# Kernel optimization log

Hardware: AMD Instinct MI355X
Metric: run time of the kernel (lower is better)

The kernel has to match this reference:

```python
import jax, jax.numpy as jnp
import numpy as np

N = 50000        # nodes
E_RAND = 800000  # random edges (self-loops appended)
H = 4            # heads
F_IN, D1, D2 = 128, 64, 64
MLP_H, NCLS = 200, 2
NEG_SLOPE = 0.2
EPS = 1e-5


def setup_inputs() -> dict:
    key = jax.random.key(0)
    ks = jax.random.split(key, 18)
    p = lambda k, shape: (jax.random.normal(k, shape, jnp.float32) * 0.05)
    features = jax.random.normal(ks[0], (N, F_IN), jnp.float32)
    loops = jnp.arange(N, dtype=jnp.int32)
    src = jnp.concatenate([jax.random.randint(ks[1], (E_RAND,), 0, N, jnp.int32), loops])
    dst = jnp.concatenate([jax.random.randint(ks[2], (E_RAND,), 0, N, jnp.int32), loops])
    return {
        "features": features, "src": src, "dst": dst,
        "W1": p(ks[3], (F_IN, H * D1)), "al1": p(ks[4], (H, D1)), "ar1": p(ks[5], (H, D1)), "b1": p(ks[6], (H * D1,)),
        "W2": p(ks[7], (D1, H * D2)), "al2": p(ks[8], (H, D2)), "ar2": p(ks[9], (H, D2)), "b2": p(ks[10], (H * D2,)),
        "Wm1": p(ks[11], (D2, MLP_H)), "bm1": p(ks[12], (MLP_H,)),
        "gamma": jnp.ones((MLP_H,), jnp.float32), "beta": jnp.zeros((MLP_H,), jnp.float32),
        "Wm2": p(ks[13], (MLP_H, NCLS)), "bm2": p(ks[14], (NCLS,)),
    }


def gat_layer(x, W, al, ar, b, src, dst):
    # x: [N, F]; W: [F, H*D]
    Hh, D = al.shape
    h = (x @ W).reshape(N, Hh, D)                      # [N,H,D]
    el = jnp.einsum('nhd,hd->nh', h, al)               # [N,H]
    er = jnp.einsum('nhd,hd->nh', h, ar)               # [N,H]
    e = jax.nn.leaky_relu(el[src] + er[dst], NEG_SLOPE)  # [E,H]
    # edge softmax over incoming edges of each dst node
    m = jax.ops.segment_max(e, dst, num_segments=N)    # [N,H]
    ex = jnp.exp(e - m[dst])
    s = jax.ops.segment_sum(ex, dst, num_segments=N)   # [N,H]
    a = ex / s[dst]                                    # [E,H]
    out = jax.ops.segment_sum(a[:, :, None] * h[src], dst, num_segments=N)  # [N,H,D]
    out = jax.nn.relu(out + b.reshape(1, Hh, D))
    return out.mean(axis=1)                            # mean over heads -> [N,D]


def reference(features, src, dst, W1, al1, ar1, b1, W2, al2, ar2, b2,
              Wm1, bm1, gamma, beta, Wm2, bm2):
    h = gat_layer(features, W1, al1, ar1, b1, src, dst)   # dropout = identity (eval)
    h = gat_layer(h, W2, al2, ar2, b2, src, dst)
    # MLPPredictor: Dropout(id) -> Linear -> ReLU -> BatchNorm1d (batch stats) -> Linear
    z = jax.nn.relu(h @ Wm1 + bm1)                        # [N, MLP_H]
    mu = z.mean(axis=0)
    var = ((z - mu) ** 2).mean(axis=0)                    # biased var (torch BN)
    z = (z - mu) * jax.lax.rsqrt(var + EPS) * gamma + beta
    return z @ Wm2 + bm2                                  # [N, NCLS]
```

## Files before the change

### kernel.cpp

```cpp
#include <hip/hip_runtime.h>
#include <hip/hip_bf16.h>

#define NNODES 50000
#define MLP_HID 200
#define NB_SCAN 196

#define NB_CONV 6250
#define NB_W1   256
#define NB_W2   256
#define NB_ZC   196
#define INIT_BLOCKS (NB_CONV + NB_W1 + NB_W2 + NB_ZC + 1)

typedef __attribute__((ext_vector_type(8))) short bf16x8;
typedef __attribute__((ext_vector_type(4))) float f32x4;

__device__ __forceinline__ unsigned short f2bf(float x){
    unsigned u = __float_as_uint(x);
    unsigned r = (u + 0x7fffu + ((u >> 16) & 1u)) >> 16;
    return (unsigned short)r;
}
__device__ __forceinline__ float bflo(unsigned u){ return __uint_as_float(u << 16); }
__device__ __forceinline__ float bfhi(unsigned u){ return __uint_as_float(u & 0xffff0000u); }

__global__ __launch_bounds__(256) void init_all(
    const float* __restrict__ feat, unsigned short* __restrict__ featbf,
    const float* __restrict__ W1, unsigned short* __restrict__ W1T,
    const float* __restrict__ W2, unsigned short* __restrict__ W2T,
    int* __restrict__ cnt, float* __restrict__ bn_acc )
{
    const int b = blockIdx.x, tid = threadIdx.x;
    if (b < NB_CONV){
        long i = ((long)b * 256 + tid) * 4;
        float4 v = *(const float4*)&feat[i];
        ushort4 p;
        p.x = f2bf(v.x); p.y = f2bf(v.y); p.z = f2bf(v.z); p.w = f2bf(v.w);
        *(ushort4*)&featbf[i] = p;
    } else if (b < NB_CONV + NB_W1){
        int c = b - NB_CONV;
        if (tid < 128) W1T[(size_t)c * 128 + tid] = f2bf(W1[(size_t)tid * 256 + c]);
    } else if (b < NB_CONV + NB_W1 + NB_W2){
        int c = b - NB_CONV - NB_W1;
        if (tid < 64) W2T[(size_t)c * 64 + tid] = f2bf(W2[(size_t)tid * 256 + c]);
    } else if (b < NB_CONV + NB_W1 + NB_W2 + NB_ZC){
        int i = (b - NB_CONV - NB_W1 - NB_W2) * 256 + tid;
        if (i < NNODES) cnt[i] = 0;
    } else {
        if (tid < 2 * MLP_HID - 256) bn_acc[256 + tid] = 0.f;
        bn_acc[tid] = 0.f;
    }
}

template<int K>
__global__ __launch_bounds__(256) void mfma_gemm_attn(
    const unsigned short* __restrict__ Abf,
    const unsigned short* __restrict__ WT,
    const float* __restrict__ al, const float* __restrict__ ar,
    unsigned short* __restrict__ hb,
    float* __restrict__ el, float* __restrict__ er, int M)
{
    const int wv = threadIdx.x >> 6, lane = threadIdx.x & 63;
    const int r0 = blockIdx.x * 64 + wv * 16;
    const int l15 = lane & 15, ks = lane >> 4;

    f32x4 acc[16];
    #pragma unroll
    for (int nt = 0; nt < 16; nt++)
        #pragma unroll
        for (int q = 0; q < 4; q++) acc[nt][q] = 0.f;

    const int arow = min(r0 + l15, M - 1);
    const unsigned short* aptr = Abf + (size_t)arow * K + ks * 8;
    const unsigned short* bptr = WT + (size_t)l15 * K + ks * 8;

    #pragma unroll
    for (int k0 = 0; k0 < K; k0 += 32){
        bf16x8 a = *(const bf16x8*)(aptr + k0);
        #pragma unroll
        for (int nt = 0; nt < 16; nt++){
            bf16x8 b = *(const bf16x8*)(bptr + (size_t)nt * 16 * K + k0);
            acc[nt] = __builtin_amdgcn_mfma_f32_16x16x32_bf16(a, b, acc[nt], 0, 0, 0);
        }
    }

    float elv[4][4], erv[4][4];
    #pragma unroll
    for (int r = 0; r < 4; r++)
        #pragma unroll
        for (int hh = 0; hh < 4; hh++){ elv[r][hh] = 0.f; erv[r][hh] = 0.f; }

    #pragma unroll
    for (int nt = 0; nt < 16; nt++){
        int col = nt * 16 + l15;
        float alv = al[col], arv = ar[col];
        #pragma unroll
        for (int reg = 0; reg < 4; reg++){
            elv[reg][nt >> 2] = fmaf(acc[nt][reg], alv, elv[reg][nt >> 2]);
            erv[reg][nt >> 2] = fmaf(acc[nt][reg], arv, erv[reg][nt >> 2]);
        }
    }
    #pragma unroll
    for (int o = 8; o > 0; o >>= 1){
        #pragma unroll
        for (int reg = 0; reg < 4; reg++)
            #pragma unroll
            for (int hh = 0; hh < 4; hh++){
                elv[reg][hh] += __shfl_xor(elv[reg][hh], o);
                erv[reg][hh] += __shfl_xor(erv[reg][hh], o);
            }
    }
    if (l15 == 0){
        #pragma unroll
        for (int reg = 0; reg < 4; reg++){
            int r = r0 + ks * 4 + reg;
            if (r < M){
                #pragma unroll
                for (int hh = 0; hh < 4; hh++){
                    el[r * 4 + hh] = elv[reg][hh];
                    er[r * 4 + hh] = erv[reg][hh];
                }
            }
        }
    }

    __shared__ __align__(16) unsigned short hbuf[4][16][264];
    #pragma unroll
    for (int nt = 0; nt < 16; nt++)
        #pragma unroll
        for (int reg = 0; reg < 4; reg++)
            hbuf[wv][ks * 4 + reg][nt * 16 + l15] = f2bf(acc[nt][reg]);
    #pragma unroll
    for (int t = 0; t < 8; t++){
        int chunk = t * 64 + lane;
        int rr = chunk >> 5;
        int cc = (chunk & 31) * 8;
        int r = r0 + rr;
        if (r < M){
            uint4 v = *(const uint4*)&hbuf[wv][rr][cc];
            *(uint4*)&hb[(size_t)r * 256 + cc] = v;
        }
    }
}

template<int KT, bool RELU, bool BN>
__global__ __launch_bounds__(256) void gemm_tile(const float* __restrict__ A,
                                                 const float* __restrict__ B,
                                                 const float* __restrict__ bias,
                                                 float* __restrict__ C,
                                                 float* __restrict__ bn_sum,
                                                 float* __restrict__ bn_sumsq,
                                                 int M, int Nc){
    __shared__ float As[16][64];
    __shared__ float Bs[16][64];
    __shared__ float bnred[16][64];
    const int tid = threadIdx.x;
    const int tx = tid & 15, ty = tid >> 4;
    const int r0 = blockIdx.y * 64, c0 = blockIdx.x * 64;
    float acc[4][4] = {};
    const int lr  = tid >> 2,  lk4 = (tid & 3) * 4;
    const int bk  = tid >> 4,  bc4 = (tid & 15) * 4;

    for (int k0 = 0; k0 < KT; k0 += 16){
        float4 av = make_float4(0.f,0.f,0.f,0.f);
        if (r0 + lr < M) av = *(const float4*)&A[(size_t)(r0 + lr) * KT + k0 + lk4];
        As[lk4+0][lr] = av.x; As[lk4+1][lr] = av.y;
        As[lk4+2][lr] = av.z; As[lk4+3][lr] = av.w;

        if (c0 + bc4 + 3 < Nc){
            float4 bv = *(const float4*)&B[(size_t)(k0 + bk) * Nc + c0 + bc4];
            Bs[bk][bc4+0] = bv.x; Bs[bk][bc4+1] = bv.y;
            Bs[bk][bc4+2] = bv.z; Bs[bk][bc4+3] = bv.w;
        } else {
            #pragma unroll
            for (int j = 0; j < 4; j++){
                int c = c0 + bc4 + j;
                Bs[bk][bc4+j] = (c < Nc) ? B[(size_t)(k0 + bk) * Nc + c] : 0.f;
            }
        }
        __syncthreads();
        #pragma unroll
        for (int kk = 0; kk < 16; kk++){
            float4 a = *(const float4*)&As[kk][ty*4];
            float4 b = *(const float4*)&Bs[kk][tx*4];
            float arr[4] = {a.x,a.y,a.z,a.w};
            float brr[4] = {b.x,b.y,b.z,b.w};
            #pragma unroll
            for (int i = 0; i < 4; i++)
                #pragma unroll
                for (int j = 0; j < 4; j++)
                    acc[i][j] = fmaf(arr[i], brr[j], acc[i][j]);
        }
        __syncthreads();
    }

    float cs[4] = {0,0,0,0}, css[4] = {0,0,0,0};
    #pragma unroll
    for (int i = 0; i < 4; i++){
        int r = r0 + ty*4 + i;
        bool rok = r < M;
        #pragma unroll
        for (int j = 0; j < 4; j++){
            int c = c0 + tx*4 + j;
            if (c >= Nc) continue;
            float v = acc[i][j];
            if (bias) v += bias[c];
            if (RELU) v = fmaxf(v, 0.f);
            if (rok){
                C[(size_t)r * Nc + c] = v;
                if (BN){ cs[j] += v; css[j] += v * v; }
            }
        }
    }
    if (BN){
        #pragma unroll
        for (int j = 0; j < 4; j++) bnred[ty][tx*4+j] = cs[j];
        __syncthreads();
        if (tid < 64){
            float s = 0.f;
            #pragma unroll
            for (int t = 0; t < 16; t++) s += bnred[t][tid];
            if (c0 + tid < Nc) atomicAdd(&bn_sum[c0 + tid], s);
        }
        __syncthreads();
        #pragma unroll
        for (int j = 0; j < 4; j++) bnred[ty][tx*4+j] = css[j];
        __syncthreads();
        if (tid < 64){
            float s = 0.f;
            #pragma unroll
            for (int t = 0; t < 16; t++) s += bnred[t][tid];
            if (c0 + tid < Nc) atomicAdd(&bn_sumsq[c0 + tid], s);
        }
    }
}

__global__ __launch_bounds__(256) void csr_count(const int* __restrict__ dst,
                                                 int* __restrict__ cnt, int E){
    int e = blockIdx.x * blockDim.x + threadIdx.x;
    if (e < E) atomicAdd(&cnt[dst[e]], 1);
}

__global__ __launch_bounds__(256) void csr_bsum(const int* __restrict__ cnt,
                                                int* __restrict__ bsum){
    __shared__ int red[256];
    int i = blockIdx.x * 256 + threadIdx.x;
    red[threadIdx.x] = (i < NNODES) ? cnt[i] : 0;
    __syncthreads();
    for (int off = 128; off > 0; off >>= 1){
        if (threadIdx.x < off) red[threadIdx.x] += red[threadIdx.x + off];
        __syncthreads();
    }
    if (threadIdx.x == 0) bsum[blockIdx.x] = red[0];
}

__global__ __launch_bounds__(256) void csr_bscan(const int* __restrict__ bsum,
                                                 int* __restrict__ boff){
    __shared__ int part[256];
    int t = threadIdx.x;
    int v = (t < NB_SCAN) ? bsum[t] : 0;
    part[t] = v;
    __syncthreads();
    for (int off = 1; off < 256; off <<= 1){
        int u = (t >= off) ? part[t - off] : 0;
        __syncthreads();
        part[t] += u;
        __syncthreads();
    }
    if (t < NB_SCAN) boff[t] = part[t] - v;
}

__global__ __launch_bounds__(256) void csr_fill(const int* __restrict__ cnt,
                                                const int* __restrict__ boff,
                                                int* __restrict__ row_ptr,
                                                int* __restrict__ cursor){
    __shared__ int part[256];
    int b = blockIdx.x, t = threadIdx.x;
    int i = b * 256 + t;
    int c = (i < NNODES) ? cnt[i] : 0;
    part[t] = c;
    __syncthreads();
    for (int off = 1; off < 256; off <<= 1){
        int u = (t >= off) ? part[t - off] : 0;
        __syncthreads();
        part[t] += u;
        __syncthreads();
    }
    int excl = part[t] - c + boff[b];
    if (i < NNODES){ row_ptr[i] = excl; cursor[i] = excl; }
    if (i == NNODES - 1) row_ptr[NNODES] = excl + c;
}

__global__ __launch_bounds__(256) void csr_scatter(const int* __restrict__ src,
                                                   const int* __restrict__ dst,
                                                   int* __restrict__ cursor,
                                                   int* __restrict__ col_src, int E){
    int e = blockIdx.x * blockDim.x + threadIdx.x;
    if (e >= E) return;
    int pos = atomicAdd(&cursor[dst[e]], 1);
    col_src[pos] = src[e];
}

__global__ __launch_bounds__(256) void gat_edge_v5(
    const int* __restrict__ row_ptr, const int* __restrict__ col_src,
    const float* __restrict__ el, const float* __restrict__ er,
    const unsigned short* __restrict__ hb, const float* __restrict__ bias,
    float* __restrict__ out_f, unsigned short* __restrict__ out_b)
{
    __shared__ float s_w[4][512];
    __shared__ int   s_idx[512];
    __shared__ float s_part[4][4];
    __shared__ float s_inv[4];
    __shared__ __align__(16) float s_red[4][264];
    __shared__ float s_val[256];

    const int n = blockIdx.x;
    const int tid = threadIdx.x;
    const int lane = tid & 63;
    const int wv = tid >> 6;
    const int rs = row_ptr[n], re = row_ptr[n + 1];
    const int K = re - rs;
    const float4 ern = *(const float4*)&er[n * 4];

    float ls0 = 0.f, ls1 = 0.f, ls2 = 0.f, ls3 = 0.f;
    for (int k = tid; k < K; k += 256){
        int s = col_src[rs + k];
        float4 e4 = *(const float4*)&el[s * 4];
        float e0 = e4.x + ern.x; e0 = (e0 >= 0.f) ? e0 : 0.2f * e0;
        float e1 = e4.y + ern.y; e1 = (e1 >= 0.f) ? e1 : 0.2f * e1;
        float e2 = e4.z + ern.z; e2 = (e2 >= 0.f) ? e2 : 0.2f * e2;
        float e3 = e4.w + ern.w; e3 = (e3 >= 0.f) ? e3 : 0.2f * e3;
        float w0 = __expf(e0), w1 = __expf(e1), w2 = __expf(e2), w3 = __expf(e3);
        if (k < 512){
            s_idx[k] = s;
            s_w[0][k] = w0; s_w[1][k] = w1; s_w[2][k] = w2; s_w[3][k] = w3;
        }
        ls0 += w0; ls1 += w1; ls2 += w2; ls3 += w3;
    }
    #pragma unroll
    for (int o = 32; o > 0; o >>= 1){
        ls0 += __shfl_xor(ls0, o); ls1 += __shfl_xor(ls1, o);
        ls2 += __shfl_xor(ls2, o); ls3 += __shfl_xor(ls3, o);
    }
    if (lane == 0){
        s_part[wv][0] = ls0; s_part[wv][1] = ls1;
        s_part[wv][2] = ls2; s_part[wv][3] = ls3;
    }
    __syncthreads();
    if (tid < 4)
        s_inv[tid] = 1.f / (s_part[0][tid] + s_part[1][tid] + s_part[2][tid] + s_part[3][tid]);
    __syncthreads();

    float acc[8];
    #pragma unroll
    for (int q = 0; q < 8; q++) acc[q] = 0.f;
    const int slot = tid >> 5;
    const int c8   = (tid & 31) * 8;
    const int hc   = c8 >> 6;

    for (int kc = 0; kc < K; kc += 512){
        if (kc > 0){
            __syncthreads();
            int kend = min(K, kc + 512);
            for (int k = kc + tid; k < kend; k += 256){
                int s = col_src[rs + k];
                float4 e4 = *(const float4*)&el[s * 4];
                float e0 = e4.x + ern.x; e0 = (e0 >= 0.f) ? e0 : 0.2f * e0;
                float e1 = e4.y + ern.y; e1 = (e1 >= 0.f) ? e1 : 0.2f * e1;
                float e2 = e4.z + ern.z; e2 = (e2 >= 0.f) ? e2 : 0.2f * e2;
                float e3 = e4.w + ern.w; e3 = (e3 >= 0.f) ? e3 : 0.2f * e3;
                int kk = k - kc;
                s_idx[kk] = s;
                s_w[0][kk] = __expf(e0); s_w[1][kk] = __expf(e1);
                s_w[2][kk] = __expf(e2); s_w[3][kk] = __expf(e3);
            }
            __syncthreads();
        }
        int rem = min(512, K - kc);
        int j = slot;
        for (; j + 8 < rem; j += 16){
            int s0 = s_idx[j], s1 = s_idx[j + 8];
            float w0 = s_w[hc][j], w1 = s_w[hc][j + 8];
            uint4 v0 = *(const uint4*)&hb[(size_t)s0 * 256 + c8];
            uint4 v1 = *(const uint4*)&hb[(size_t)s1 * 256 + c8];
            acc[0] = fmaf(w0, bflo(v0.x), acc[0]);
            acc[1] = fmaf(w0, bfhi(v0.x), acc[1]);
            acc[2] = fmaf(w0, bflo(v0.y), acc[2]);
            acc[3] = fmaf(w0, bfhi(v0.y), acc[3]);
            acc[4] = fmaf(w0, bflo(v0.z), acc[4]);
            acc[5] = fmaf(w0, bfhi(v0.z), acc[5]);
            acc[6] = fmaf(w0, bflo(v0.w), acc[6]);
            acc[7] = fmaf(w0, bfhi(v0.w), acc[7]);
            acc[0] = fmaf(w1, bflo(v1.x), acc[0]);
            acc[1] = fmaf(w1, bfhi(v1.x), acc[1]);
            acc[2] = fmaf(w1, bflo(v1.y), acc[2]);
            acc[3] = fmaf(w1, bfhi(v1.y), acc[3]);
            acc[4] = fmaf(w1, bflo(v1.z), acc[4]);
            acc[5] = fmaf(w1, bfhi(v1.z), acc[5]);
            acc[6] = fmaf(w1, bflo(v1.w), acc[6]);
            acc[7] = fmaf(w1, bfhi(v1.w), acc[7]);
        }
        if (j < rem){
            int sN = s_idx[j];
            float w = s_w[hc][j];
            uint4 v = *(const uint4*)&hb[(size_t)sN * 256 + c8];
            acc[0] = fmaf(w, bflo(v.x), acc[0]);
            acc[1] = fmaf(w, bfhi(v.x), acc[1]);
            acc[2] = fmaf(w, bflo(v.y), acc[2]);
            acc[3] = fmaf(w, bfhi(v.y), acc[3]);
            acc[4] = fmaf(w, bflo(v.z), acc[4]);
            acc[5] = fmaf(w, bfhi(v.z), acc[5]);
            acc[6] = fmaf(w, bflo(v.w), acc[6]);
            acc[7] = fmaf(w, bfhi(v.w), acc[7]);
        }
    }
    const float invh = s_inv[hc];
    #pragma unroll
    for (int q = 0; q < 8; q++) acc[q] = acc[q] * invh + __shfl_xor(acc[q] * invh, 32);

    if ((tid & 32) == 0){
        *(float4*)&s_red[slot >> 1][c8]     = make_float4(acc[0], acc[1], acc[2], acc[3]);
        *(float4*)&s_red[slot >> 1][c8 + 4] = make_float4(acc[4], acc[5], acc[6], acc[7]);
    }
    __syncthreads();
    {
        int d = tid;
        float v = s_red[0][d] + s_red[1][d] + s_red[2][d] + s_red[3][d];
        v = fmaxf(v + bias[d], 0.f);
        s_val[d] = v;
    }
    __syncthreads();
    if (tid < 64){
        float m = (s_val[tid] + s_val[tid + 64] + s_val[tid + 128] + s_val[tid + 192]) * 0.25f;
        if (out_f) out_f[(size_t)n * 64 + tid] = m;
        out_b[(size_t)n * 64 + tid] = f2bf(m);
    }
}

__global__ void bn_final(const float* __restrict__ bsum,
                         const float* __restrict__ bsumsq,
                         const float* __restrict__ gamma,
                         const float* __restrict__ beta,
                         float* __restrict__ scale,
                         float* __restrict__ shift,
                         int Nrows){
    int col = threadIdx.x;
    if (col >= MLP_HID) return;
    float inv = 1.f / (float)Nrows;
    float mu = bsum[col] * inv;
    float var = bsumsq[col] * inv - mu * mu;
    float rstd = rsqrtf(var + 1e-5f);
    float sc = rstd * gamma[col];
    scale[col] = sc;
    shift[col] = beta[col] - mu * sc;
}

__global__ __launch_bounds__(256) void mlp2(const float* __restrict__ z,
                                            const float* __restrict__ scale,
                                            const float* __restrict__ shift,
                                            const float* __restrict__ Wm2,
                                            const float* __restrict__ bm2,
                                            float* __restrict__ out,
                                            int Nrows){
    int g = blockIdx.x * blockDim.x + threadIdx.x;
    int n = g >> 6;
    if (n >= Nrows) return;
    int lane = threadIdx.x & 63;
    float a0 = 0.f, a1 = 0.f;
    for (int k = lane; k < MLP_HID; k += 64){
        float zn = z[(size_t)n * MLP_HID + k] * scale[k] + shift[k];
        a0 = fmaf(zn, Wm2[k * 2 + 0], a0);
        a1 = fmaf(zn, Wm2[k * 2 + 1], a1);
    }
    #pragma unroll
    for (int o = 32; o > 0; o >>= 1){
        a0 += __shfl_xor(a0, o);
        a1 += __shfl_xor(a1, o);
    }
    if (lane == 0){
        out[n * 2 + 0] = a0 + bm2[0];
        out[n * 2 + 1] = a1 + bm2[1];
    }
}

extern "C" void kernel_launch(void* const* d_in, const int* in_sizes, int n_in,
                              void* d_out, int out_size, void* d_ws, size_t ws_size,
                              hipStream_t stream) {
    const float* feat  = (const float*)d_in[0];
    const int*   src   = (const int*)  d_in[1];
    const int*   dst   = (const int*)  d_in[2];
    const float* W1    = (const float*)d_in[3];
    const float* al1   = (const float*)d_in[4];
    const float* ar1   = (const float*)d_in[5];
    const float* b1    = (const float*)d_in[6];
    const float* W2    = (const float*)d_in[7];
    const float* al2   = (const float*)d_in[8];
    const float* ar2   = (const float*)d_in[9];
    const float* b2    = (const float*)d_in[10];
    const float* Wm1   = (const float*)d_in[11];
    const float* bm1   = (const float*)d_in[12];
    const float* gamma = (const float*)d_in[13];
    const float* beta  = (const float*)d_in[14];
    const float* Wm2   = (const float*)d_in[15];
    const float* bm2   = (const float*)d_in[16];
    const int E = in_sizes[1];
    float* out = (float*)d_out;

    unsigned short* h_bf   = (unsigned short*)d_ws;
    unsigned short* featbf = h_bf   + (size_t)NNODES * 256;
    unsigned short* o1_bf  = featbf + (size_t)NNODES * 128;
    unsigned short* o2_bf  = o1_bf  + (size_t)NNODES * 64;
    unsigned short* W1T    = o2_bf  + (size_t)NNODES * 64;
    unsigned short* W2T    = W1T + 256 * 128;
    float* z      = (float*)(W2T + 256 * 64);
    float* el     = z      + (size_t)NNODES * MLP_HID;
    float* er     = el     + (size_t)NNODES * 4;
    float* bn_sum   = er + (size_t)NNODES * 4;
    float* bn_sumsq = bn_sum + MLP_HID;
    float* bn_scale = bn_sumsq + MLP_HID;
    float* bn_shift = bn_scale + MLP_HID;
    int* cnt      = (int*)(bn_shift + MLP_HID);
    int* row_ptr  = cnt + NNODES;
    int* cursor   = row_ptr + NNODES + 1;
    int* bsum     = cursor + NNODES;
    int* boff     = bsum + 256;
    int* col_src  = boff + 256;
    float* out2_f = (float*)featbf;

    const dim3 blk(256);
    const int eg = (E + 255) / 256;
    const int gb = (NNODES + 63) / 64;

    init_all<<<INIT_BLOCKS, blk, 0, stream>>>(feat, featbf, W1, W1T, W2, W2T,
                                              cnt, bn_sum);

    csr_count<<<eg, blk, 0, stream>>>(dst, cnt, E);
    csr_bsum<<<NB_SCAN, blk, 0, stream>>>(cnt, bsum);
    csr_bscan<<<1, blk, 0, stream>>>(bsum, boff);
    csr_fill<<<NB_SCAN, blk, 0, stream>>>(cnt, boff, row_ptr, cursor);
    csr_scatter<<<eg, blk, 0, stream>>>(src, dst, cursor, col_src, E);

    mfma_gemm_attn<128><<<gb, blk, 0, stream>>>(featbf, W1T, al1, ar1, h_bf, el, er, NNODES);
    gat_edge_v5<<<NNODES, blk, 0, stream>>>(row_ptr, col_src, el, er, h_bf, b1,
                                            nullptr, o1_bf);

    mfma_gemm_attn<64><<<gb, blk, 0, stream>>>(o1_bf, W2T, al2, ar2, h_bf, el, er, NNODES);
    gat_edge_v5<<<NNODES, blk, 0, stream>>>(row_ptr, col_src, el, er, h_bf, b2,
                                            out2_f, o2_bf);

    gemm_tile<64,true,true><<<dim3((MLP_HID + 63) / 64, gb), blk, 0, stream>>>(
        out2_f, Wm1, bm1, z, bn_sum, bn_sumsq, NNODES, MLP_HID);

    bn_final<<<1, 256, 0, stream>>>(bn_sum, bn_sumsq, gamma, beta, bn_scale, bn_shift, NNODES);
    mlp2<<<(NNODES * 64 + 255) / 256, blk, 0, stream>>>(
        z, bn_scale, bn_shift, Wm2, bm2, out, NNODES);
}
```

Measured before the change: 427.4 us.

## Process one destination node per wavefront in GAT edge kernel and fold BN finalize into mlp2

The edge aggregation kernel now maps each destination node to a single 64-lane wavefront, with four nodes per block, instead of giving each node a whole 256-thread block. This removes the block-wide __syncthreads and shared-memory reductions, doing the softmax sum and the head-mean reduction with wave shuffles and vectorized output stores. With about 17 edges per node, most of the old block sat idle. The separate bn_final launch is removed and each mlp2 block recomputes the BN scale and shift into shared memory, which trades one kernel launch for redundant per-block work. Each wave now does all of a node's gather work, so high-degree nodes serialize more within a wave.

```diff
diff --git a/kernel.cpp b/kernel.cpp
--- a/kernel.cpp
+++ b/kernel.cpp
@@ -4,6 +4,7 @@
 #define NNODES 50000
 #define MLP_HID 200
 #define NB_SCAN 196
+#define CAP 128
 
 #define NB_CONV 6250
 #define NB_W1   256
@@ -299,29 +300,28 @@
     col_src[pos] = src[e];
 }
 
-__global__ __launch_bounds__(256) void gat_edge_v5(
+__global__ __launch_bounds__(256) void gat_edge_v6(
     const int* __restrict__ row_ptr, const int* __restrict__ col_src,
     const float* __restrict__ el, const float* __restrict__ er,
     const unsigned short* __restrict__ hb, const float* __restrict__ bias,
-    float* __restrict__ out_f, unsigned short* __restrict__ out_b)
+    float* __restrict__ out_f, unsigned short* __restrict__ out_b, int N)
 {
-    __shared__ float s_w[4][512];
-    __shared__ int   s_idx[512];
-    __shared__ float s_part[4][4];
-    __shared__ float s_inv[4];
-    __shared__ __align__(16) float s_red[4][264];
-    __shared__ float s_val[256];
-
-    const int n = blockIdx.x;
-    const int tid = threadIdx.x;
-    const int lane = tid & 63;
-    const int wv = tid >> 6;
+    __shared__ float s_w[4][4][132];
+    __shared__ int   s_idx[4][CAP];
+
+    const int wv = threadIdx.x >> 6;
+    const int lane = threadIdx.x & 63;
+    const int n = blockIdx.x * 4 + wv;
+    if (n >= N) return;
+
     const int rs = row_ptr[n], re = row_ptr[n + 1];
     const int K = re - rs;
     const float4 ern = *(const float4*)&er[n * 4];
+    float (*sw)[132] = s_w[wv];
+    int* sidx = s_idx[wv];
 
     float ls0 = 0.f, ls1 = 0.f, ls2 = 0.f, ls3 = 0.f;
-    for (int k = tid; k < K; k += 256){
+    for (int k = lane; k < K; k += 64){
         int s = col_src[rs + k];
         float4 e4 = *(const float4*)&el[s * 4];
         float e0 = e4.x + ern.x; e0 = (e0 >= 0.f) ? e0 : 0.2f * e0;
@@ -329,9 +329,9 @@
         float e2 = e4.z + ern.z; e2 = (e2 >= 0.f) ? e2 : 0.2f * e2;
         float e3 = e4.w + ern.w; e3 = (e3 >= 0.f) ? e3 : 0.2f * e3;
         float w0 = __expf(e0), w1 = __expf(e1), w2 = __expf(e2), w3 = __expf(e3);
-        if (k < 512){
-            s_idx[k] = s;
-            s_w[0][k] = w0; s_w[1][k] = w1; s_w[2][k] = w2; s_w[3][k] = w3;
+        if (k < CAP){
+            sidx[k] = s;
+            sw[0][k] = w0; sw[1][k] = w1; sw[2][k] = w2; sw[3][k] = w3;
         }
         ls0 += w0; ls1 += w1; ls2 += w2; ls3 += w3;
     }
@@ -340,133 +340,119 @@
         ls0 += __shfl_xor(ls0, o); ls1 += __shfl_xor(ls1, o);
         ls2 += __shfl_xor(ls2, o); ls3 += __shfl_xor(ls3, o);
     }
-    if (lane == 0){
-        s_part[wv][0] = ls0; s_part[wv][1] = ls1;
-        s_part[wv][2] = ls2; s_part[wv][3] = ls3;
-    }
-    __syncthreads();
-    if (tid < 4)
-        s_inv[tid] = 1.f / (s_part[0][tid] + s_part[1][tid] + s_part[2][tid] + s_part[3][tid]);
-    __syncthreads();
+    const int slot = lane >> 5;
+    const int c8   = (lane & 31) * 8;
+    const int hc   = c8 >> 6;
+    const float invh = 1.f / (hc == 0 ? ls0 : hc == 1 ? ls1 : hc == 2 ? ls2 : ls3);
 
     float acc[8];
     #pragma unroll
     for (int q = 0; q < 8; q++) acc[q] = 0.f;
-    const int slot = tid >> 5;
-    const int c8   = (tid & 31) * 8;
-    const int hc   = c8 >> 6;
-
-    for (int kc = 0; kc < K; kc += 512){
-        if (kc > 0){
-            __syncthreads();
-            int kend = min(K, kc + 512);
-            for (int k = kc + tid; k < kend; k += 256){
+
+    for (int base = 0; base < K; base += CAP){
+        if (base > 0){
+            for (int k = base + lane; k < min(K, base + CAP); k += 64){
                 int s = col_src[rs + k];
                 float4 e4 = *(const float4*)&el[s * 4];
                 float e0 = e4.x + ern.x; e0 = (e0 >= 0.f) ? e0 : 0.2f * e0;
                 float e1 = e4.y + ern.y; e1 = (e1 >= 0.f) ? e1 : 0.2f * e1;
                 float e2 = e4.z + ern.z; e2 = (e2 >= 0.f) ? e2 : 0.2f * e2;
                 float e3 = e4.w + ern.w; e3 = (e3 >= 0.f) ? e3 : 0.2f * e3;
-                int kk = k - kc;
-                s_idx[kk] = s;
-                s_w[0][kk] = __expf(e0); s_w[1][kk] = __expf(e1);
-                s_w[2][kk] = __expf(e2); s_w[3][kk] = __expf(e3);
+                int kk = k - base;
+                sidx[kk] = s;
+                sw[0][kk] = __expf(e0); sw[1][kk] = __expf(e1);
+                sw[2][kk] = __expf(e2); sw[3][kk] = __expf(e3);
             }
-            __syncthreads();
-        }
-        int rem = min(512, K - kc);
+        }
+        const int rem = min(CAP, K - base);
         int j = slot;
-        for (; j + 8 < rem; j += 16){
-            int s0 = s_idx[j], s1 = s_idx[j + 8];
-            float w0 = s_w[hc][j], w1 = s_w[hc][j + 8];
-            uint4 v0 = *(const uint4*)&hb[(size_t)s0 * 256 + c8];
-            uint4 v1 = *(const uint4*)&hb[(size_t)s1 * 256 + c8];
-            acc[0] = fmaf(w0, bflo(v0.x), acc[0]);
-            acc[1] = fmaf(w0, bfhi(v0.x), acc[1]);
-            acc[2] = fmaf(w0, bflo(v0.y), acc[2]);
-            acc[3] = fmaf(w0, bfhi(v0.y), acc[3]);
-            acc[4] = fmaf(w0, bflo(v0.z), acc[4]);
-            acc[5] = fmaf(w0, bfhi(v0.z), acc[5]);
-            acc[6] = fmaf(w0, bflo(v0.w), acc[6]);
-            acc[7] = fmaf(w0, bfhi(v0.w), acc[7]);
-            acc[0] = fmaf(w1, bflo(v1.x), acc[0]);
-            acc[1] = fmaf(w1, bfhi(v1.x), acc[1]);
-            acc[2] = fmaf(w1, bflo(v1.y), acc[2]);
-            acc[3] = fmaf(w1, bfhi(v1.y), acc[3]);
-            acc[4] = fmaf(w1, bflo(v1.z), acc[4]);
-            acc[5] = fmaf(w1, bfhi(v1.z), acc[5]);
-            acc[6] = fmaf(w1, bflo(v1.w), acc[6]);
-            acc[7] = fmaf(w1, bfhi(v1.w), acc[7]);
+        for (; j + 2 < rem; j += 4){
+            int   sA = sidx[j],     sB = sidx[j + 2];
+            float wA = sw[hc][j],   wB = sw[hc][j + 2];
+            uint4 vA = *(const uint4*)&hb[(size_t)sA * 256 + c8];
+            uint4 vB = *(const uint4*)&hb[(size_t)sB * 256 + c8];
+            acc[0] = fmaf(wA, bflo(vA.x), acc[0]);
+            acc[1] = fmaf(wA, bfhi(vA.x), acc[1]);
+            acc[2] = fmaf(wA, bflo(vA.y), acc[2]);
+            acc[3] = fmaf(wA, bfhi(vA.y), acc[3]);
+            acc[4] = fmaf(wA, bflo(vA.z), acc[4]);
+            acc[5] = fmaf(wA, bfhi(vA.z), acc[5]);
+            acc[6] = fmaf(wA, bflo(vA.w), acc[6]);
+            acc[7] = fmaf(wA, bfhi(vA.w), acc[7]);
+            acc[0] = fmaf(wB, bflo(vB.x), acc[0]);
+            acc[1] = fmaf(wB, bfhi(vB.x), acc[1]);
+            acc[2] = fmaf(wB, bflo(vB.y), acc[2]);
+            acc[3] = fmaf(wB, bfhi(vB.y), acc[3]);
+            acc[4] = fmaf(wB, bflo(vB.z), acc[4]);
+            acc[5] = fmaf(wB, bfhi(vB.z), acc[5]);
+            acc[6] = fmaf(wB, bflo(vB.w), acc[6]);
+            acc[7] = fmaf(wB, bfhi(vB.w), acc[7]);
         }
         if (j < rem){
-            int sN = s_idx[j];
-            float w = s_w[hc][j];
-            uint4 v = *(const uint4*)&hb[(size_t)sN * 256 + c8];
-            acc[0] = fmaf(w, bflo(v.x), acc[0]);
-            acc[1] = fmaf(w, bfhi(v.x), acc[1]);
-            acc[2] = fmaf(w, bflo(v.y), acc[2]);
-            acc[3] = fmaf(w, bfhi(v.y), acc[3]);
-            acc[4] = fmaf(w, bflo(v.z), acc[4]);
-            acc[5] = fmaf(w, bfhi(v.z), acc[5]);
-            acc[6] = fmaf(w, bflo(v.w), acc[6]);
-            acc[7] = fmaf(w, bfhi(v.w), acc[7]);
-        }
-    }
-    const float invh = s_inv[hc];
-    #pragma unroll
-    for (int q = 0; q < 8; q++) acc[q] = acc[q] * invh + __shfl_xor(acc[q] * invh, 32);
-
-    if ((tid & 32) == 0){
-        *(float4*)&s_red[slot >> 1][c8]     = make_float4(acc[0], acc[1], acc[2], acc[3]);
-        *(float4*)&s_red[slot >> 1][c8 + 4] = make_float4(acc[4], acc[5], acc[6], acc[7]);
-    }
-    __syncthreads();
-    {
-        int d = tid;
-        float v = s_red[0][d] + s_red[1][d] + s_red[2][d] + s_red[3][d];
-        v = fmaxf(v + bias[d], 0.f);
-        s_val[d] = v;
-    }
-    __syncthreads();
-    if (tid < 64){
-        float m = (s_val[tid] + s_val[tid + 64] + s_val[tid + 128] + s_val[tid + 192]) * 0.25f;
-        if (out_f) out_f[(size_t)n * 64 + tid] = m;
-        out_b[(size_t)n * 64 + tid] = f2bf(m);
-    }
-}
-
-__global__ void bn_final(const float* __restrict__ bsum,
-                         const float* __restrict__ bsumsq,
-                         const float* __restrict__ gamma,
-                         const float* __restrict__ beta,
-                         float* __restrict__ scale,
-                         float* __restrict__ shift,
-                         int Nrows){
-    int col = threadIdx.x;
-    if (col >= MLP_HID) return;
-    float inv = 1.f / (float)Nrows;
-    float mu = bsum[col] * inv;
-    float var = bsumsq[col] * inv - mu * mu;
-    float rstd = rsqrtf(var + 1e-5f);
-    float sc = rstd * gamma[col];
-    scale[col] = sc;
-    shift[col] = beta[col] - mu * sc;
+            int   sA = sidx[j];
+            float wA = sw[hc][j];
+            uint4 vA = *(const uint4*)&hb[(size_t)sA * 256 + c8];
+            acc[0] = fmaf(wA, bflo(vA.x), acc[0]);
+            acc[1] = fmaf(wA, bfhi(vA.x), acc[1]);
+            acc[2] = fmaf(wA, bflo(vA.y), acc[2]);
+            acc[3] = fmaf(wA, bfhi(vA.y), acc[3]);
+            acc[4] = fmaf(wA, bflo(vA.z), acc[4]);
+            acc[5] = fmaf(wA, bfhi(vA.z), acc[5]);
+            acc[6] = fmaf(wA, bflo(vA.w), acc[6]);
+            acc[7] = fmaf(wA, bfhi(vA.w), acc[7]);
+        }
+    }
+
+    #pragma unroll
+    for (int q = 0; q < 8; q++){
+        acc[q] *= invh;
+        acc[q] += __shfl_xor(acc[q], 32);
+        acc[q] = fmaxf(acc[q] + bias[c8 + q], 0.f);
+        acc[q] += __shfl_xor(acc[q], 8);
+        acc[q] += __shfl_xor(acc[q], 16);
+        acc[q] *= 0.25f;
+    }
+    if (lane < 8){
+        uint4 pb;
+        pb.x = (unsigned)f2bf(acc[0]) | ((unsigned)f2bf(acc[1]) << 16);
+        pb.y = (unsigned)f2bf(acc[2]) | ((unsigned)f2bf(acc[3]) << 16);
+        pb.z = (unsigned)f2bf(acc[4]) | ((unsigned)f2bf(acc[5]) << 16);
+        pb.w = (unsigned)f2bf(acc[6]) | ((unsigned)f2bf(acc[7]) << 16);
+        *(uint4*)&out_b[(size_t)n * 64 + lane * 8] = pb;
+        if (out_f){
+            *(float4*)&out_f[(size_t)n * 64 + lane * 8]     = make_float4(acc[0], acc[1], acc[2], acc[3]);
+            *(float4*)&out_f[(size_t)n * 64 + lane * 8 + 4] = make_float4(acc[4], acc[5], acc[6], acc[7]);
+        }
+    }
 }
 
 __global__ __launch_bounds__(256) void mlp2(const float* __restrict__ z,
-                                            const float* __restrict__ scale,
-                                            const float* __restrict__ shift,
+                                            const float* __restrict__ bn_sum,
+                                            const float* __restrict__ bn_sumsq,
+                                            const float* __restrict__ gamma,
+                                            const float* __restrict__ beta,
                                             const float* __restrict__ Wm2,
                                             const float* __restrict__ bm2,
                                             float* __restrict__ out,
                                             int Nrows){
-    int g = blockIdx.x * blockDim.x + threadIdx.x;
-    int n = g >> 6;
+    __shared__ float s_scale[MLP_HID], s_shift[MLP_HID];
+    const int tid = threadIdx.x;
+    if (tid < MLP_HID){
+        float inv = 1.f / (float)Nrows;
+        float mu = bn_sum[tid] * inv;
+        float var = bn_sumsq[tid] * inv - mu * mu;
+        float rstd = rsqrtf(var + 1e-5f);
+        float sc = rstd * gamma[tid];
+        s_scale[tid] = sc;
+        s_shift[tid] = beta[tid] - mu * sc;
+    }
+    __syncthreads();
+    int n = (blockIdx.x * 256 + tid) >> 6;
     if (n >= Nrows) return;
-    int lane = threadIdx.x & 63;
+    int lane = tid & 63;
     float a0 = 0.f, a1 = 0.f;
     for (int k = lane; k < MLP_HID; k += 64){
-        float zn = z[(size_t)n * MLP_HID + k] * scale[k] + shift[k];
+        float zn = z[(size_t)n * MLP_HID + k] * s_scale[k] + s_shift[k];
         a0 = fmaf(zn, Wm2[k * 2 + 0], a0);
         a1 = fmaf(zn, Wm2[k * 2 + 1], a1);
     }
@@ -515,9 +501,7 @@
     float* er     = el     + (size_t)NNODES * 4;
     float* bn_sum   = er + (size_t)NNODES * 4;
     float* bn_sumsq = bn_sum + MLP_HID;
-    float* bn_scale = bn_sumsq + MLP_HID;
-    float* bn_shift = bn_scale + MLP_HID;
-    int* cnt      = (int*)(bn_shift + MLP_HID);
+    int* cnt      = (int*)(bn_sumsq + MLP_HID);
     int* row_ptr  = cnt + NNODES;
     int* cursor   = row_ptr + NNODES + 1;
     int* bsum     = cursor + NNODES;
@@ -528,6 +512,7 @@
     const dim3 blk(256);
     const int eg = (E + 255) / 256;
     const int gb = (NNODES + 63) / 64;
+    const int ng4 = (NNODES + 3) / 4;
 
     init_all<<<INIT_BLOCKS, blk, 0, stream>>>(feat, featbf, W1, W1T, W2, W2T,
                                               cnt, bn_sum);
@@ -539,17 +524,16 @@
     csr_scatter<<<eg, blk, 0, stream>>>(src, dst, cursor, col_src, E);
 
     mfma_gemm_attn<128><<<gb, blk, 0, stream>>>(featbf, W1T, al1, ar1, h_bf, el, er, NNODES);
-    gat_edge_v5<<<NNODES, blk, 0, stream>>>(row_ptr, col_src, el, er, h_bf, b1,
-                                            nullptr, o1_bf);
+    gat_edge_v6<<<ng4, blk, 0, stream>>>(row_ptr, col_src, el, er, h_bf, b1,
+                                         nullptr, o1_bf, NNODES);
 
     mfma_gemm_attn<64><<<gb, blk, 0, stream>>>(o1_bf, W2T, al2, ar2, h_bf, el, er, NNODES);
-    gat_edge_v5<<<NNODES, blk, 0, stream>>>(row_ptr, col_src, el, er, h_bf, b2,
-                                            out2_f, o2_bf);
+    gat_edge_v6<<<ng4, blk, 0, stream>>>(row_ptr, col_src, el, er, h_bf, b2,
+                                         out2_f, o2_bf, NNODES);
 
     gemm_tile<64,true,true><<<dim3((MLP_HID + 63) / 64, gb), blk, 0, stream>>>(
         out2_f, Wm1, bm1, z, bn_sum, bn_sumsq, NNODES, MLP_HID);
 
-    bn_final<<<1, 256, 0, stream>>>(bn_sum, bn_sumsq, gamma, beta, bn_scale, bn_shift, NNODES);
     mlp2<<<(NNODES * 64 + 255) / 256, blk, 0, stream>>>(
-        z, bn_scale, bn_shift, Wm2, bm2, out, NNODES);
-}
+        z, bn_sum, bn_sumsq, gamma, beta, Wm2, bm2, out, NNODES);
+}
```

Measured after the change: 378.3 us. -11.5%, faster.
